# Kernel tuning notes

Hardware: AMD Instinct MI355X
Metric: run time of the kernel (lower is better)

The kernel has to match this reference:

```python
import jax, jax.numpy as jnp
import numpy as np

EMBED_DIM = 1024
NUM_HEADS = 16
HEAD_DIM = EMBED_DIM // NUM_HEADS
B, T = 2, 2048


def setup_inputs() -> dict:
    key = jax.random.key(0)
    ks = jax.random.split(key, 10)
    s_in = 1.0 / np.sqrt(EMBED_DIM)
    s_hd = 1.0 / np.sqrt(HEAD_DIM)
    return {
        "hidden_states": jax.random.normal(ks[0], (B, T, EMBED_DIM), jnp.float32),
        "attn_mask": jnp.zeros((T, T), jnp.float32),
        # per-head parameter stacks (nn.Linear: y = x @ W^T + b); store W pre-transposed
        "W_q": jax.random.uniform(ks[1], (NUM_HEADS, EMBED_DIM, HEAD_DIM), jnp.float32, -s_in, s_in),
        "b_q": jax.random.uniform(ks[2], (NUM_HEADS, HEAD_DIM), jnp.float32, -s_in, s_in),
        "W_k": jax.random.uniform(ks[3], (NUM_HEADS, EMBED_DIM, HEAD_DIM), jnp.float32, -s_in, s_in),
        "b_k": jax.random.uniform(ks[4], (NUM_HEADS, HEAD_DIM), jnp.float32, -s_in, s_in),
        "W_v": jax.random.uniform(ks[5], (NUM_HEADS, EMBED_DIM, HEAD_DIM), jnp.float32, -s_in, s_in),
        "b_v": jax.random.uniform(ks[6], (NUM_HEADS, HEAD_DIM), jnp.float32, -s_in, s_in),
        "W_o": jax.random.uniform(ks[7], (NUM_HEADS, HEAD_DIM, EMBED_DIM), jnp.float32, -s_hd, s_hd),
        "b_o": jax.random.uniform(ks[8], (NUM_HEADS, EMBED_DIM), jnp.float32, -s_hd, s_hd),
        "gate": jnp.ones((NUM_HEADS,), jnp.float32),
    }


def reference(hidden_states, attn_mask, W_q, b_q, W_k, b_k, W_v, b_v, W_o, b_o, gate):
    # All heads: state='active', consent=True (defaults); dropout in eval mode.
    scale = 1.0 / np.sqrt(HEAD_DIM)
    # Q,K,V: [B,H,T,hd]
    Q = jnp.einsum("btd,hde->bhte", hidden_states, W_q) + b_q[None, :, None, :]
    K = jnp.einsum("btd,hde->bhte", hidden_states, W_k) + b_k[None, :, None, :]
    V = jnp.einsum("btd,hde->bhte", hidden_states, W_v) + b_v[None, :, None, :]
    scores = jnp.einsum("bhte,bhse->bhts", Q, K) * scale + attn_mask[None, None, :, :]
    weights = jax.nn.softmax(scores, axis=-1)
    out = jnp.einsum("bhts,bhse->bhte", weights, V)  # [B,H,T,hd]
    # per-head scalar norm: mean over (B,T) of L2 norm along head_dim, floored at 1e-5
    denom = jnp.maximum(
        jnp.sqrt(jnp.sum(out * out, axis=-1)).mean(axis=(0, 2)), 1e-5
    )  # [H]
    out_n = out / denom[None, :, None, None]
    g = jnp.clip(gate, 0.0, 1.0)  # gate_factor = 1.0 for 'active' heads
    # projected per head: (out_n @ W_o + b_o) * g; then sum over heads / H
    proj = (jnp.einsum("bhte,hed->bhtd", out_n, W_o) + b_o[None, :, None, :]) * g[None, :, None, None]
    return proj.sum(axis=1) / NUM_HEADS
```

## Files before the change

kernel.cpp:

```cpp
#include <hip/hip_runtime.h>
#include <hip/hip_bf16.h>
#include <math.h>

#define EMBED_DIM 1024
#define NUM_HEADS 16
#define HEAD_DIM  64
#define B_SZ      2
#define T_SZ      2048
#define BT        (B_SZ * T_SZ)
#define LOG2E     1.44269504088896340736f
#define QSCALE    (0.125f * LOG2E)
#define SOFT_OFF  8.0f

typedef short bf16x8 __attribute__((ext_vector_type(8)));
typedef float f32x4  __attribute__((ext_vector_type(4)));

#define MFMA16(a, b, c) __builtin_amdgcn_mfma_f32_16x16x32_bf16((a), (b), (c), 0, 0, 0)

__device__ inline short f2bf(float f) {
    unsigned u = __builtin_bit_cast(unsigned, f);
    u = (u + 0x7fffu + ((u >> 16) & 1u)) >> 16;
    return (short)u;
}
__device__ inline float bf2f(short s) {
    unsigned u = ((unsigned)(unsigned short)s) << 16;
    return __builtin_bit_cast(float, u);
}
__device__ inline unsigned pk2(float a, float b) {
#if __has_builtin(__builtin_amdgcn_cvt_pk_bf16_f32)
    typedef __bf16 bf2_t __attribute__((ext_vector_type(2)));
    bf2_t t = __builtin_amdgcn_cvt_pk_bf16_f32(a, b);
    return __builtin_bit_cast(unsigned, t);
#else
    return (unsigned)(unsigned short)f2bf(a) | ((unsigned)(unsigned short)f2bf(b) << 16);
#endif
}

__device__ inline float ex2(float x) {
#if __has_builtin(__builtin_amdgcn_exp2f)
    return __builtin_amdgcn_exp2f(x);
#else
    return exp2f(x);
#endif
}

__device__ inline void gld16(const short* g, short* lds) {
    __builtin_amdgcn_global_load_lds(
        (const __attribute__((address_space(1))) void*)g,
        (__attribute__((address_space(3))) void*)lds, 16, 0, 0);
}

__device__ inline bf16x8 frag_swz(const short* tile, int R, int C) {
    return *(const bf16x8*)(tile + R * 64 + ((C ^ (R & 7)) << 3));
}

__device__ inline float red_add64(float v) {
    v += __shfl_xor(v, 1); v += __shfl_xor(v, 2); v += __shfl_xor(v, 4);
    v += __shfl_xor(v, 8); v += __shfl_xor(v, 16); v += __shfl_xor(v, 32);
    return v;
}

__global__ __launch_bounds__(256) void prep_kernel(
    const float* __restrict__ hs, short* __restrict__ hsb,
    const float* __restrict__ maskf, unsigned* __restrict__ flagsW,
    const float* __restrict__ Wq, const float* __restrict__ Wk,
    const float* __restrict__ Wv, const float* __restrict__ Wo,
    short* __restrict__ Wqt, short* __restrict__ Wkt,
    short* __restrict__ Wvt, short* __restrict__ WoT)
{
    __shared__ float tile[32][33];
    const int bx = blockIdx.x, tid = threadIdx.x;

    if (bx < 4096) {
        const long i = ((long)bx * 256 + tid) * 4;
        const float4 v = *(const float4*)(hs + i);
        ushort4 o; o.x = f2bf(v.x); o.y = f2bf(v.y); o.z = f2bf(v.z); o.w = f2bf(v.w);
        *(ushort4*)(hsb + i) = o;
    } else if (bx < 4608) {
        const int flat = bx - 4096;
        const int qc = flat >> 5, kt = flat & 31;
        const float* base = maskf + (long)qc * 128 * 2048 + kt * 64;
        unsigned u = 0;
        #pragma unroll
        for (int i = 0; i < 8; ++i) {
            const int f2 = i * 256 + tid;
            const int r = f2 >> 4, c4 = f2 & 15;
            const uint4 v = *(const uint4*)(base + (long)r * 2048 + c4 * 4);
            u |= v.x | v.y | v.z | v.w;
        }
        if (__any(u != 0) && (tid & 63) == 0)
            atomicOr(&flagsW[qc], 1u << kt);
    } else {
        const int j = bx - 4608;
        const int x = j & 63, rest = j >> 6;
        const int h = rest & 15, arr = rest >> 4;
        const float* src; short* dst; int R, C;
        if (arr == 0)      { src = Wq; dst = Wqt; R = 1024; C = 64; }
        else if (arr == 1) { src = Wk; dst = Wkt; R = 1024; C = 64; }
        else if (arr == 2) { src = Wv; dst = Wvt; R = 1024; C = 64; }
        else               { src = Wo; dst = WoT; R = 64;   C = 1024; }
        src += (long)h * 65536; dst += (long)h * 65536;

        const int ct = C / 32;
        const int tr = x / ct, tc = x % ct;
        const int tx = tid & 31, ty = tid >> 5;
        #pragma unroll
        for (int i = 0; i < 4; ++i) {
            const int r = ty + 8 * i;
            tile[r][tx] = src[(long)(tr * 32 + r) * C + tc * 32 + tx];
        }
        __syncthreads();
        #pragma unroll
        for (int i = 0; i < 4; ++i) {
            const int r = ty + 8 * i;
            dst[(long)(tc * 32 + r) * R + tr * 32 + tx] = f2bf(tile[tx][r]);
        }
    }
}

__global__ __launch_bounds__(256) void qkv_mfma_kernel(
    const short* __restrict__ hsb,
    const short* __restrict__ Wt,
    const float* __restrict__ bq, const float* __restrict__ bk,
    const float* __restrict__ bv,
    short* __restrict__ Qb, short* __restrict__ Kb, short* __restrict__ Vtb)
{
    const int r_ = blockIdx.x;
    const int c_ = r_ & 7, j_ = r_ >> 3;
    const int xi = j_ & 7, yi = j_ >> 3;
    const int m0 = ((c_ & 3) * 8 + xi) * 128;
    const int n0 = ((c_ >> 2) * 12 + yi) * 128;
    const int type = n0 >> 10;

    __shared__ short As[128 * 64];
    __shared__ short Bs[128 * 64];

    const int tid = threadIdx.x, lane = tid & 63, w = tid >> 6;
    const int wm = w & 1, wn = w >> 1;
    const int quad = lane >> 4, l15 = lane & 15;

    f32x4 acc[4][4] = {};

    if (type < 2) {
        for (int k0 = 0; k0 < 1024; k0 += 64) {
            __syncthreads();
            #pragma unroll
            for (int t = 0; t < 4; ++t) {
                const int r0 = w * 32 + t * 8;
                const int r  = r0 + (lane >> 3);
                const int cg = (lane & 7) ^ (r & 7);
                gld16(hsb + (long)(m0 + r) * 1024 + k0 + cg * 8, &As[r0 * 64]);
                gld16(Wt  + (long)(n0 + r) * 1024 + k0 + cg * 8, &Bs[r0 * 64]);
            }
            __syncthreads();
            #pragma unroll
            for (int ks = 0; ks < 2; ++ks) {
                bf16x8 af[4];
                #pragma unroll
                for (int ms = 0; ms < 4; ++ms)
                    af[ms] = frag_swz(As, wm * 64 + ms * 16 + l15, ks * 4 + quad);
                #pragma unroll
                for (int ns = 0; ns < 4; ++ns) {
                    const bf16x8 bfr = frag_swz(Bs, wn * 64 + ns * 16 + l15, ks * 4 + quad);
                    #pragma unroll
                    for (int ms = 0; ms < 4; ++ms)
                        acc[ms][ns] = MFMA16(bfr, af[ms], acc[ms][ns]);
                }
            }
        }

        const int hh = (((n0 + wn * 64) >> 6) & 15);
        const float* bsrc = (type == 0 ? bq : bk) + hh * 64;
        short* dst = (type == 0 ? Qb : Kb);
        const float sc = (type == 0) ? QSCALE : 1.0f;
        #pragma unroll
        for (int ns = 0; ns < 4; ++ns) {
            const int e0 = ns * 16 + quad * 4;
            const float4 b4 = *(const float4*)(bsrc + e0);
            #pragma unroll
            for (int ms = 0; ms < 4; ++ms) {
                const int t  = m0 + wm * 64 + ms * 16 + l15;
                const int bb = t >> 11, t0 = t & 2047;
                ushort4 pk;
                pk.x = (unsigned short)f2bf((acc[ms][ns][0] + b4.x) * sc);
                pk.y = (unsigned short)f2bf((acc[ms][ns][1] + b4.y) * sc);
                pk.z = (unsigned short)f2bf((acc[ms][ns][2] + b4.z) * sc);
                pk.w = (unsigned short)f2bf((acc[ms][ns][3] + b4.w) * sc);
                *(ushort4*)&dst[((long)(bb * 16 + hh) * 2048 + t0) * 64 + e0] = pk;
            }
        }
    } else {
        for (int k0 = 0; k0 < 1024; k0 += 64) {
            __syncthreads();
            #pragma unroll
            for (int t = 0; t < 4; ++t) {
                const int r0 = w * 32 + t * 8;
                const int r  = r0 + (lane >> 3);
                const int cg = (lane & 7) ^ (r & 7);
                gld16(hsb + (long)(m0 + r) * 1024 + k0 + cg * 8, &As[r0 * 64]);
                gld16(Wt  + (long)(n0 + r) * 1024 + k0 + cg * 8, &Bs[r0 * 64]);
            }
            __syncthreads();
            #pragma unroll
            for (int ks = 0; ks < 2; ++ks) {
                bf16x8 af[4];
                #pragma unroll
                for (int ms = 0; ms < 4; ++ms)
                    af[ms] = frag_swz(As, wm * 64 + ms * 16 + l15, ks * 4 + quad);
                #pragma unroll
                for (int ns = 0; ns < 4; ++ns) {
                    const bf16x8 bfr = frag_swz(Bs, wn * 64 + ns * 16 + l15, ks * 4 + quad);
                    #pragma unroll
                    for (int ms = 0; ms < 4; ++ms)
                        acc[ms][ns] = MFMA16(af[ms], bfr, acc[ms][ns]);
                }
            }
        }

        #pragma unroll
        for (int ns = 0; ns < 4; ++ns) {
            const int n = n0 + wn * 64 + ns * 16 + l15;
            const int h = (n >> 6) & 15;
            const int e = n & 63;
            const float bias = bv[h * 64 + e];
            #pragma unroll
            for (int ms = 0; ms < 4; ++ms) {
                const int mbase = m0 + wm * 64 + ms * 16 + quad * 4;
                const int bb = mbase >> 11, t0 = mbase & 2047;
                const int tp = (t0 & ~63) | (t0 & 35) | ((t0 & 12) << 1) | ((t0 & 16) >> 2);
                ushort4 pk;
                pk.x = (unsigned short)f2bf(acc[ms][ns][0] + bias);
                pk.y = (unsigned short)f2bf(acc[ms][ns][1] + bias);
                pk.z = (unsigned short)f2bf(acc[ms][ns][2] + bias);
                pk.w = (unsigned short)f2bf(acc[ms][ns][3] + bias);
                *(ushort4*)&Vtb[((long)(bb * 16 + h) * 64 + e) * 2048 + tp] = pk;
            }
        }
    }
}

__global__ __launch_bounds__(512) void attn_mfma_kernel(
    const short* __restrict__ Qb, const short* __restrict__ Kb,
    const short* __restrict__ Vtb, const float* __restrict__ maskf,
    const unsigned* __restrict__ flagsW,
    short* __restrict__ Ob, float* __restrict__ denomsum)
{
    const int r_  = blockIdx.x;
    const int c_  = r_ & 7, j_ = r_ >> 3;
    const int g_  = c_ + 8 * (j_ >> 4);
    const int qc  = j_ & 15;
    const int q0  = qc * 128;
    const int h   = g_ & 15, b = g_ >> 4;
    const long bh = ((long)b * 16 + h) * (long)T_SZ * 64;

    __shared__ short Ks[2][128 * 64];
    __shared__ short Vs[2][128 * 64];
    __shared__ float wred[8];

    const int tid = threadIdx.x, lane = tid & 63, w = tid >> 6;
    const int quad = lane >> 4, l15 = lane & 15;
    const int qrow = q0 + w * 16 + l15;

    const unsigned zf = flagsW[qc];

    const short* Kg = Kb + bh;
    const short* Vg = Vtb + bh;

    bf16x8 qf[2];
    #pragma unroll
    for (int ks = 0; ks < 2; ++ks)
        qf[ks] = *(const bf16x8*)(Qb + bh + (long)qrow * 64 + ks * 32 + quad * 8);

    bf16x8 ones;
    #pragma unroll
    for (int i = 0; i < 8; ++i) ones[i] = (short)0x3F80;

    f32x4 o[4] = {};
    f32x4 lacc = {};

    const float* mrow = maskf + (long)qrow * 2048 + quad * 4;

    auto stageKV = [&](int st, int buf) {
        const int kv0 = st * 128;
        #pragma unroll
        for (int t = 0; t < 2; ++t) {
            const int r0 = w * 16 + t * 8;
            const int r  = r0 + (lane >> 3);
            const int cg = (lane & 7) ^ (r & 7);
            gld16(Kg + (long)(kv0 + r) * 64 + cg * 8, &Ks[buf][r0 * 64]);
        }
        #pragma unroll
        for (int t = 0; t < 2; ++t) {
            const int r0 = w * 8;
            const int r  = r0 + (lane >> 3);
            const int cg = (lane & 7) ^ (r & 7);
            gld16(Vg + (long)r * 2048 + kv0 + t * 64 + cg * 8,
                  &Vs[buf][t * 4096 + r0 * 64]);
        }
    };

    stageKV(0, 0);

    for (int st = 0; st < 16; ++st) {
        const int cur = st & 1;

        __builtin_amdgcn_s_barrier();
        asm volatile("" ::: "memory");
        if (st < 15) {
            stageKV(st + 1, cur ^ 1);
            asm volatile("s_waitcnt vmcnt(4)" ::: "memory");
        } else {
            asm volatile("s_waitcnt vmcnt(0)" ::: "memory");
        }
        __builtin_amdgcn_s_barrier();
        asm volatile("" ::: "memory");

        #pragma unroll
        for (int k2 = 0; k2 < 2; ++k2) {
            const int kt = st * 2 + k2;
            const short* Kt = &Ks[cur][k2 * 4096];
            const short* Vt = &Vs[cur][k2 * 4096];

            f32x4 s[4];
            if (zf & (1u << kt)) {
                const int kv0 = kt * 64;
                #pragma unroll
                for (int kb = 0; kb < 4; ++kb) {
                    const float4 m = *(const float4*)(mrow + kv0 + kb * 16);
                    s[kb][0] = fmaf(m.x, LOG2E, -SOFT_OFF);
                    s[kb][1] = fmaf(m.y, LOG2E, -SOFT_OFF);
                    s[kb][2] = fmaf(m.z, LOG2E, -SOFT_OFF);
                    s[kb][3] = fmaf(m.w, LOG2E, -SOFT_OFF);
                }
            } else {
                #pragma unroll
                for (int kb = 0; kb < 4; ++kb) {
                    s[kb][0] = -SOFT_OFF; s[kb][1] = -SOFT_OFF;
                    s[kb][2] = -SOFT_OFF; s[kb][3] = -SOFT_OFF;
                }
            }

            __builtin_amdgcn_s_setprio(1);
            #pragma unroll
            for (int ks = 0; ks < 2; ++ks)
                #pragma unroll
                for (int kb = 0; kb < 4; ++kb) {
                    const bf16x8 kf = frag_swz(Kt, kb * 16 + l15, ks * 4 + quad);
                    s[kb] = MFMA16(kf, qf[ks], s[kb]);
                }
            __builtin_amdgcn_s_setprio(0);

            unsigned w0[4], w1[4];
            #pragma unroll
            for (int kb = 0; kb < 4; ++kb) {
                const float p0 = ex2(s[kb][0]);
                const float p1 = ex2(s[kb][1]);
                const float p2 = ex2(s[kb][2]);
                const float p3 = ex2(s[kb][3]);
                w0[kb] = pk2(p0, p1);
                w1[kb] = pk2(p2, p3);
            }

            __builtin_amdgcn_s_setprio(1);
            #pragma unroll
            for (int kbp = 0; kbp < 2; ++kbp) {
                const uint4 u = {w0[2 * kbp], w1[2 * kbp],
                                 w0[2 * kbp + 1], w1[2 * kbp + 1]};
                const bf16x8 pb = __builtin_bit_cast(bf16x8, u);
                lacc = MFMA16(ones, pb, lacc);
                #pragma unroll
                for (int eb = 0; eb < 4; ++eb) {
                    const bf16x8 va = frag_swz(Vt, eb * 16 + l15, kbp * 4 + quad);
                    o[eb] = MFMA16(va, pb, o[eb]);
                }
            }
            __builtin_amdgcn_s_setprio(0);
        }
    }

    const float inv = 1.f / lacc[0];
    float ss = 0.f;
    #pragma unroll
    for (int eb = 0; eb < 4; ++eb) {
        o[eb] *= inv;
        #pragma unroll
        for (int r = 0; r < 4; ++r) ss += o[eb][r] * o[eb][r];
    }
    ss += __shfl_xor(ss, 16);
    ss += __shfl_xor(ss, 32);
    const float tot = sqrtf(ss);

    #pragma unroll
    for (int eb = 0; eb < 4; ++eb) {
        uint2 pk;
        pk.x = pk2(o[eb][0], o[eb][1]);
        pk.y = pk2(o[eb][2], o[eb][3]);
        *(uint2*)&Ob[((long)(b * 2048 + qrow)) * 1024 + h * 64 + eb * 16 + quad * 4] = pk;
    }

    const float wsum = red_add64(tot) * 0.25f;
    if (lane == 0) wred[w] = wsum;
    __syncthreads();
    if (tid == 0) {
        float acc = 0.f;
        #pragma unroll
        for (int i = 0; i < 8; ++i) acc += wred[i];
        atomicAdd(&denomsum[h], acc);
    }
}

__global__ __launch_bounds__(256) void scale_w_kernel(
    short* __restrict__ WoT, const float* __restrict__ denomsum,
    const float* __restrict__ gate)
{
    __shared__ float sh[16];
    if (threadIdx.x < 16) {
        const float g  = fminf(fmaxf(gate[threadIdx.x], 0.f), 1.f);
        const float dn = fmaxf(denomsum[threadIdx.x] * (1.f / (float)BT), 1e-5f);
        sh[threadIdx.x] = g / (dn * (float)NUM_HEADS);
    }
    __syncthreads();
    const long i = ((long)blockIdx.x * 256 + threadIdx.x) * 4;
    const float sc = sh[(int)(i >> 16)];
    ushort4 v = *(ushort4*)(WoT + i);
    v.x = (unsigned short)f2bf(bf2f((short)v.x) * sc);
    v.y = (unsigned short)f2bf(bf2f((short)v.y) * sc);
    v.z = (unsigned short)f2bf(bf2f((short)v.z) * sc);
    v.w = (unsigned short)f2bf(bf2f((short)v.w) * sc);
    *(ushort4*)(WoT + i) = v;
}

__global__ __launch_bounds__(256) void oproj_mfma_kernel(
    const short* __restrict__ Ob,
    const short* __restrict__ WoT,
    const float* __restrict__ bo,
    const float* __restrict__ gate,
    float* __restrict__ out)
{
    const int m0 = blockIdx.x * 64;
    const int n0 = blockIdx.y * 128;
    __shared__ short As[2][64 * 64];
    __shared__ short Bs[2][128 * 64];

    const int tid = threadIdx.x, lane = tid & 63, w = tid >> 6;
    const int wm = w & 1, wn = w >> 1;
    const int quad = lane >> 4, l15 = lane & 15;

    auto stage = [&](int h, int buf) {
        #pragma unroll
        for (int t = 0; t < 2; ++t) {
            const int r0 = w * 16 + t * 8;
            const int r  = r0 + (lane >> 3);
            const int cg = (lane & 7) ^ (r & 7);
            gld16(Ob + (long)(m0 + r) * 1024 + h * 64 + cg * 8, &As[buf][r0 * 64]);
        }
        #pragma unroll
        for (int t = 0; t < 4; ++t) {
            const int r0 = w * 32 + t * 8;
            const int r  = r0 + (lane >> 3);
            const int cg = (lane & 7) ^ (r & 7);
            gld16(WoT + (long)h * 65536 + (long)(n0 + r) * 64 + cg * 8, &Bs[buf][r0 * 64]);
        }
    };

    f32x4 acc[2][4] = {};
    stage(0, 0);

    for (int h = 0; h < 16; ++h) {
        const int cur = h & 1;
        __syncthreads();
        if (h < 15) stage(h + 1, cur ^ 1);
        #pragma unroll
        for (int ks = 0; ks < 2; ++ks) {
            bf16x8 af[2];
            #pragma unroll
            for (int ms = 0; ms < 2; ++ms)
                af[ms] = frag_swz(&As[cur][0], wm * 32 + ms * 16 + l15, ks * 4 + quad);
            #pragma unroll
            for (int ns = 0; ns < 4; ++ns) {
                const bf16x8 bfr = frag_swz(&Bs[cur][0], wn * 64 + ns * 16 + l15, ks * 4 + quad);
                #pragma unroll
                for (int ms = 0; ms < 2; ++ms)
                    acc[ms][ns] = MFMA16(af[ms], bfr, acc[ms][ns]);
            }
        }
    }

    float gcl[16];
    #pragma unroll
    for (int hh = 0; hh < 16; ++hh)
        gcl[hh] = fminf(fmaxf(gate[hh], 0.f), 1.f) * (1.f / (float)NUM_HEADS);

    #pragma unroll
    for (int ns = 0; ns < 4; ++ns) {
        const int n = n0 + wn * 64 + ns * 16 + l15;
        float be = 0.f;
        #pragma unroll
        for (int hh = 0; hh < 16; ++hh) be += gcl[hh] * bo[hh * 1024 + n];
        #pragma unroll
        for (int ms = 0; ms < 2; ++ms) {
            const int m = m0 + wm * 32 + ms * 16 + quad * 4;
            #pragma unroll
            for (int r = 0; r < 4; ++r)
                out[(long)(m + r) * 1024 + n] = acc[ms][ns][r] + be;
        }
    }
}

extern "C" void kernel_launch(void* const* d_in, const int* in_sizes, int n_in,
                              void* d_out, int out_size, void* d_ws, size_t ws_size,
                              hipStream_t stream)
{
    const float* hs   = (const float*)d_in[0];
    const float* mask = (const float*)d_in[1];
    const float* Wq   = (const float*)d_in[2];
    const float* bq   = (const float*)d_in[3];
    const float* Wk   = (const float*)d_in[4];
    const float* bk   = (const float*)d_in[5];
    const float* Wv   = (const float*)d_in[6];
    const float* bv   = (const float*)d_in[7];
    const float* Wo   = (const float*)d_in[8];
    const float* bo   = (const float*)d_in[9];
    const float* gate = (const float*)d_in[10];
    float* out = (float*)d_out;

    char* ws = (char*)d_ws;
    const size_t MB = 1024 * 1024;
    short* hsb   = (short*)(ws);
    short* Wqt   = (short*)(ws + 8  * MB);
    short* Wkt   = (short*)(ws + 10 * MB);
    short* Wvt   = (short*)(ws + 12 * MB);
    short* WoT   = (short*)(ws + 14 * MB);
    short* Qb    = (short*)(ws + 16 * MB);
    short* Kb    = (short*)(ws + 24 * MB);
    short* Vtb   = (short*)(ws + 32 * MB);
    short* Ob    = (short*)(ws + 40 * MB);
    float* denomsum = (float*)(ws + 48 * MB);
    unsigned* flagsW = (unsigned*)(ws + 48 * MB + 4096);

    (void)hipMemsetAsync(denomsum, 0, NUM_HEADS * sizeof(float), stream);
    (void)hipMemsetAsync(flagsW, 0, 16 * sizeof(unsigned), stream);

    prep_kernel<<<8704, 256, 0, stream>>>(
        hs, hsb, mask, flagsW, Wq, Wk, Wv, Wo, Wqt, Wkt, Wvt, WoT);
    qkv_mfma_kernel<<<768, 256, 0, stream>>>(
        hsb, Wqt, bq, bk, bv, Qb, Kb, Vtb);
    attn_mfma_kernel<<<512, 512, 0, stream>>>(
        Qb, Kb, Vtb, mask, flagsW, Ob, denomsum);
    scale_w_kernel<<<1024, 256, 0, stream>>>(WoT, denomsum, gate);
    oproj_mfma_kernel<<<dim3(64, 8), 256, 0, stream>>>(
        Ob, WoT, bo, gate, out);
}
```

Measured before the change: 221.2 us.

## Split attention KV range in two halves and add combine kernel

The attention kernel now splits each query tile's key/value range into two halves, launching twice as many blocks with smaller LDS tiles. Each half writes unnormalized bf16 partial outputs and row sums, and a new combine kernel merges them, normalizes, writes Ob and accumulates the per-head norm sums. The aim is more parallelism and occupancy on the many-CU GPU. The cost is an extra launch, extra global traffic for the partials, and bf16 rounding of the unnormalized partials. Opart reuses the hsb workspace region, which the qkv kernel no longer needs at that point.

```diff
diff --git a/kernel.cpp b/kernel.cpp
--- a/kernel.cpp
+++ b/kernel.cpp
@@ -52,12 +52,6 @@
 
 __device__ inline bf16x8 frag_swz(const short* tile, int R, int C) {
     return *(const bf16x8*)(tile + R * 64 + ((C ^ (R & 7)) << 3));
-}
-
-__device__ inline float red_add64(float v) {
-    v += __shfl_xor(v, 1); v += __shfl_xor(v, 2); v += __shfl_xor(v, 4);
-    v += __shfl_xor(v, 8); v += __shfl_xor(v, 16); v += __shfl_xor(v, 32);
-    return v;
 }
 
 __global__ __launch_bounds__(256) void prep_kernel(
@@ -243,19 +237,21 @@
     const short* __restrict__ Qb, const short* __restrict__ Kb,
     const short* __restrict__ Vtb, const float* __restrict__ maskf,
     const unsigned* __restrict__ flagsW,
-    short* __restrict__ Ob, float* __restrict__ denomsum)
-{
-    const int r_  = blockIdx.x;
-    const int c_  = r_ & 7, j_ = r_ >> 3;
-    const int g_  = c_ + 8 * (j_ >> 4);
-    const int qc  = j_ & 15;
-    const int q0  = qc * 128;
-    const int h   = g_ & 15, b = g_ >> 4;
-    const long bh = ((long)b * 16 + h) * (long)T_SZ * 64;
-
-    __shared__ short Ks[2][128 * 64];
-    __shared__ short Vs[2][128 * 64];
-    __shared__ float wred[8];
+    short* __restrict__ Opart,
+    float* __restrict__ lpart)
+{
+    const int r_   = blockIdx.x;
+    const int c_   = r_ & 7, j_ = r_ >> 3;
+    const int hb   = c_ + 8 * (j_ >> 5);
+    const int qh   = j_ & 31;
+    const int qc   = qh & 15, half = qh >> 4;
+    const int q0   = qc * 128;
+    const int h    = hb & 15, b = hb >> 4;
+    const long bh  = ((long)b * 16 + h) * (long)T_SZ * 64;
+    const int kvbase = half * 1024;
+
+    __shared__ short Ks[2][64 * 64];
+    __shared__ short Vs[2][64 * 64];
 
     const int tid = threadIdx.x, lane = tid & 63, w = tid >> 6;
     const int quad = lane >> 4, l15 = lane & 15;
@@ -278,135 +274,135 @@
     f32x4 o[4] = {};
     f32x4 lacc = {};
 
-    const float* mrow = maskf + (long)qrow * 2048 + quad * 4;
-
-    auto stageKV = [&](int st, int buf) {
-        const int kv0 = st * 128;
-        #pragma unroll
-        for (int t = 0; t < 2; ++t) {
-            const int r0 = w * 16 + t * 8;
-            const int r  = r0 + (lane >> 3);
-            const int cg = (lane & 7) ^ (r & 7);
-            gld16(Kg + (long)(kv0 + r) * 64 + cg * 8, &Ks[buf][r0 * 64]);
-        }
-        #pragma unroll
-        for (int t = 0; t < 2; ++t) {
-            const int r0 = w * 8;
-            const int r  = r0 + (lane >> 3);
-            const int cg = (lane & 7) ^ (r & 7);
-            gld16(Vg + (long)r * 2048 + kv0 + t * 64 + cg * 8,
-                  &Vs[buf][t * 4096 + r0 * 64]);
-        }
+    const float* mrow = maskf + (long)qrow * 2048 + kvbase + quad * 4;
+
+    auto stageKV = [&](int kt, int buf) {
+        const int kv0 = kvbase + kt * 64;
+        const int r0 = w * 8;
+        const int r  = r0 + (lane >> 3);
+        const int cg = (lane & 7) ^ (r & 7);
+        gld16(Kg + (long)(kv0 + r) * 64 + cg * 8, &Ks[buf][r0 * 64]);
+        gld16(Vg + (long)r * 2048 + kv0 + cg * 8, &Vs[buf][r0 * 64]);
     };
 
     stageKV(0, 0);
 
-    for (int st = 0; st < 16; ++st) {
-        const int cur = st & 1;
+    for (int kt = 0; kt < 16; ++kt) {
+        const int cur = kt & 1;
 
         __builtin_amdgcn_s_barrier();
         asm volatile("" ::: "memory");
-        if (st < 15) {
-            stageKV(st + 1, cur ^ 1);
-            asm volatile("s_waitcnt vmcnt(4)" ::: "memory");
+        if (kt < 15) {
+            stageKV(kt + 1, cur ^ 1);
+            asm volatile("s_waitcnt vmcnt(2)" ::: "memory");
         } else {
             asm volatile("s_waitcnt vmcnt(0)" ::: "memory");
         }
         __builtin_amdgcn_s_barrier();
         asm volatile("" ::: "memory");
 
-        #pragma unroll
-        for (int k2 = 0; k2 < 2; ++k2) {
-            const int kt = st * 2 + k2;
-            const short* Kt = &Ks[cur][k2 * 4096];
-            const short* Vt = &Vs[cur][k2 * 4096];
-
-            f32x4 s[4];
-            if (zf & (1u << kt)) {
-                const int kv0 = kt * 64;
-                #pragma unroll
-                for (int kb = 0; kb < 4; ++kb) {
-                    const float4 m = *(const float4*)(mrow + kv0 + kb * 16);
-                    s[kb][0] = fmaf(m.x, LOG2E, -SOFT_OFF);
-                    s[kb][1] = fmaf(m.y, LOG2E, -SOFT_OFF);
-                    s[kb][2] = fmaf(m.z, LOG2E, -SOFT_OFF);
-                    s[kb][3] = fmaf(m.w, LOG2E, -SOFT_OFF);
-                }
-            } else {
-                #pragma unroll
-                for (int kb = 0; kb < 4; ++kb) {
-                    s[kb][0] = -SOFT_OFF; s[kb][1] = -SOFT_OFF;
-                    s[kb][2] = -SOFT_OFF; s[kb][3] = -SOFT_OFF;
-                }
-            }
-
-            __builtin_amdgcn_s_setprio(1);
-            #pragma unroll
-            for (int ks = 0; ks < 2; ++ks)
-                #pragma unroll
-                for (int kb = 0; kb < 4; ++kb) {
-                    const bf16x8 kf = frag_swz(Kt, kb * 16 + l15, ks * 4 + quad);
-                    s[kb] = MFMA16(kf, qf[ks], s[kb]);
-                }
-            __builtin_amdgcn_s_setprio(0);
-
-            unsigned w0[4], w1[4];
+        f32x4 s[4];
+        if (zf & (1u << (half * 16 + kt))) {
+            const int kv0 = kt * 64;
             #pragma unroll
             for (int kb = 0; kb < 4; ++kb) {
-                const float p0 = ex2(s[kb][0]);
-                const float p1 = ex2(s[kb][1]);
-                const float p2 = ex2(s[kb][2]);
-                const float p3 = ex2(s[kb][3]);
-                w0[kb] = pk2(p0, p1);
-                w1[kb] = pk2(p2, p3);
-            }
-
-            __builtin_amdgcn_s_setprio(1);
-            #pragma unroll
-            for (int kbp = 0; kbp < 2; ++kbp) {
-                const uint4 u = {w0[2 * kbp], w1[2 * kbp],
-                                 w0[2 * kbp + 1], w1[2 * kbp + 1]};
-                const bf16x8 pb = __builtin_bit_cast(bf16x8, u);
-                lacc = MFMA16(ones, pb, lacc);
-                #pragma unroll
-                for (int eb = 0; eb < 4; ++eb) {
-                    const bf16x8 va = frag_swz(Vt, eb * 16 + l15, kbp * 4 + quad);
-                    o[eb] = MFMA16(va, pb, o[eb]);
-                }
-            }
-            __builtin_amdgcn_s_setprio(0);
-        }
-    }
-
-    const float inv = 1.f / lacc[0];
-    float ss = 0.f;
-    #pragma unroll
-    for (int eb = 0; eb < 4; ++eb) {
-        o[eb] *= inv;
-        #pragma unroll
-        for (int r = 0; r < 4; ++r) ss += o[eb][r] * o[eb][r];
-    }
-    ss += __shfl_xor(ss, 16);
-    ss += __shfl_xor(ss, 32);
-    const float tot = sqrtf(ss);
-
+                const float4 m = *(const float4*)(mrow + kv0 + kb * 16);
+                s[kb][0] = fmaf(m.x, LOG2E, -SOFT_OFF);
+                s[kb][1] = fmaf(m.y, LOG2E, -SOFT_OFF);
+                s[kb][2] = fmaf(m.z, LOG2E, -SOFT_OFF);
+                s[kb][3] = fmaf(m.w, LOG2E, -SOFT_OFF);
+            }
+        } else {
+            #pragma unroll
+            for (int kb = 0; kb < 4; ++kb) {
+                s[kb][0] = -SOFT_OFF; s[kb][1] = -SOFT_OFF;
+                s[kb][2] = -SOFT_OFF; s[kb][3] = -SOFT_OFF;
+            }
+        }
+
+        __builtin_amdgcn_s_setprio(1);
+        #pragma unroll
+        for (int ks = 0; ks < 2; ++ks)
+            #pragma unroll
+            for (int kb = 0; kb < 4; ++kb) {
+                const bf16x8 kf = frag_swz(&Ks[cur][0], kb * 16 + l15, ks * 4 + quad);
+                s[kb] = MFMA16(kf, qf[ks], s[kb]);
+            }
+        __builtin_amdgcn_s_setprio(0);
+
+        unsigned w0[4], w1[4];
+        #pragma unroll
+        for (int kb = 0; kb < 4; ++kb) {
+            const float p0 = ex2(s[kb][0]);
+            const float p1 = ex2(s[kb][1]);
+            const float p2 = ex2(s[kb][2]);
+            const float p3 = ex2(s[kb][3]);
+            w0[kb] = pk2(p0, p1);
+            w1[kb] = pk2(p2, p3);
+        }
+
+        __builtin_amdgcn_s_setprio(1);
+        #pragma unroll
+        for (int kbp = 0; kbp < 2; ++kbp) {
+            const uint4 u = {w0[2 * kbp], w1[2 * kbp],
+                             w0[2 * kbp + 1], w1[2 * kbp + 1]};
+            const bf16x8 pb = __builtin_bit_cast(bf16x8, u);
+            lacc = MFMA16(ones, pb, lacc);
+            #pragma unroll
+            for (int eb = 0; eb < 4; ++eb) {
+                const bf16x8 va = frag_swz(&Vs[cur][0], eb * 16 + l15, kbp * 4 + quad);
+                o[eb] = MFMA16(va, pb, o[eb]);
+            }
+        }
+        __builtin_amdgcn_s_setprio(0);
+    }
+
+    const long rbase = (long)b * 2048 + qrow;
     #pragma unroll
     for (int eb = 0; eb < 4; ++eb) {
         uint2 pk;
         pk.x = pk2(o[eb][0], o[eb][1]);
         pk.y = pk2(o[eb][2], o[eb][3]);
-        *(uint2*)&Ob[((long)(b * 2048 + qrow)) * 1024 + h * 64 + eb * 16 + quad * 4] = pk;
-    }
-
-    const float wsum = red_add64(tot) * 0.25f;
-    if (lane == 0) wred[w] = wsum;
+        *(uint2*)&Opart[(long)half * (4096 * 1024) + rbase * 1024 +
+                        h * 64 + eb * 16 + quad * 4] = pk;
+    }
+    if (quad == 0)
+        lpart[(long)half * (4096 * 16) + rbase * 16 + h] = lacc[0];
+}
+
+__global__ __launch_bounds__(256) void combine_kernel(
+    const short* __restrict__ Opart,
+    const float* __restrict__ lpart,
+    short* __restrict__ Ob,
+    float* __restrict__ denomsum)
+{
+    __shared__ float hacc[16];
+    const int tid = threadIdx.x;
+    if (tid < 16) hacc[tid] = 0.f;
     __syncthreads();
-    if (tid == 0) {
-        float acc = 0.f;
-        #pragma unroll
-        for (int i = 0; i < 8; ++i) acc += wred[i];
-        atomicAdd(&denomsum[h], acc);
-    }
+    const int h = tid >> 4;
+    const int row0 = blockIdx.x * 8;
+    for (int rr = 0; rr < 8; ++rr) {
+        const int row = row0 + rr;
+        const long base = (long)row * 1024 + tid * 4;
+        const ushort4 a0 = *(const ushort4*)(Opart + base);
+        const ushort4 a1 = *(const ushort4*)(Opart + (long)4096 * 1024 + base);
+        const float l0 = lpart[row * 16 + h];
+        const float l1 = lpart[4096 * 16 + row * 16 + h];
+        const float inv = 1.f / (l0 + l1);
+        const float o0 = (bf2f((short)a0.x) + bf2f((short)a1.x)) * inv;
+        const float o1 = (bf2f((short)a0.y) + bf2f((short)a1.y)) * inv;
+        const float o2 = (bf2f((short)a0.z) + bf2f((short)a1.z)) * inv;
+        const float o3 = (bf2f((short)a0.w) + bf2f((short)a1.w)) * inv;
+        uint2 pk; pk.x = pk2(o0, o1); pk.y = pk2(o2, o3);
+        *(uint2*)(Ob + base) = pk;
+        float ss = (o0 * o0 + o1 * o1) + (o2 * o2 + o3 * o3);
+        ss += __shfl_xor(ss, 1); ss += __shfl_xor(ss, 2);
+        ss += __shfl_xor(ss, 4); ss += __shfl_xor(ss, 8);
+        if ((tid & 15) == 0) atomicAdd(&hacc[h], sqrtf(ss));
+    }
+    __syncthreads();
+    if (tid < 16) atomicAdd(&denomsum[tid], hacc[tid]);
 }
 
 __global__ __launch_bounds__(256) void scale_w_kernel(
@@ -530,13 +526,15 @@
     short* Wqt   = (short*)(ws + 8  * MB);
     short* Wkt   = (short*)(ws + 10 * MB);
     short* Wvt   = (short*)(ws + 12 * MB);
-    short* WoT   = (short*)(ws + 14 * MB);
+    short* Opart = (short*)(ws);
     short* Qb    = (short*)(ws + 16 * MB);
     short* Kb    = (short*)(ws + 24 * MB);
     short* Vtb   = (short*)(ws + 32 * MB);
     short* Ob    = (short*)(ws + 40 * MB);
-    float* denomsum = (float*)(ws + 48 * MB);
-    unsigned* flagsW = (unsigned*)(ws + 48 * MB + 4096);
+    short* WoT   = (short*)(ws + 48 * MB);
+    float* lpart = (float*)(ws + 50 * MB);
+    float* denomsum = (float*)(ws + 51 * MB);
+    unsigned* flagsW = (unsigned*)(ws + 51 * MB + 4096);
 
     (void)hipMemsetAsync(denomsum, 0, NUM_HEADS * sizeof(float), stream);
     (void)hipMemsetAsync(flagsW, 0, 16 * sizeof(unsigned), stream);
@@ -545,8 +543,9 @@
         hs, hsb, mask, flagsW, Wq, Wk, Wv, Wo, Wqt, Wkt, Wvt, WoT);
     qkv_mfma_kernel<<<768, 256, 0, stream>>>(
         hsb, Wqt, bq, bk, bv, Qb, Kb, Vtb);
-    attn_mfma_kernel<<<512, 512, 0, stream>>>(
-        Qb, Kb, Vtb, mask, flagsW, Ob, denomsum);
+    attn_mfma_kernel<<<1024, 512, 0, stream>>>(
+        Qb, Kb, Vtb, mask, flagsW, Opart, lpart);
+    combine_kernel<<<512, 256, 0, stream>>>(Opart, lpart, Ob, denomsum);
     scale_w_kernel<<<1024, 256, 0, stream>>>(WoT, denomsum, gate);
     oproj_mfma_kernel<<<dim3(64, 8), 256, 0, stream>>>(
         Ob, WoT, bo, gate, out);
```

Result: slower. 238.4 us (+7.8%).

## Fold per-head norm scaling into output projection and drop scale_w kernel

Applied to the files above, without the earlier changes.

Removes the separate scale_w_kernel launch, which rescaled the bf16 Wo weights by gate/denominator. The output projection now applies that per-head scale to a per-head partial accumulator inside the K loop. Wo is re-laid out as a single [1024 x 1024] matrix with heads concatenated along K. Block tiling changes from 64x128 to 128x64, and the double-buffered LDS staging is replaced by a single buffer with two barriers per step. This trades the loss of load/compute overlap and extra FMAs per head for one fewer launch and less weight memory traffic.

```diff
diff --git a/kernel.cpp b/kernel.cpp
--- a/kernel.cpp
+++ b/kernel.cpp
@@ -66,7 +66,7 @@
     const float* __restrict__ Wq, const float* __restrict__ Wk,
     const float* __restrict__ Wv, const float* __restrict__ Wo,
     short* __restrict__ Wqt, short* __restrict__ Wkt,
-    short* __restrict__ Wvt, short* __restrict__ WoT)
+    short* __restrict__ Wvt, short* __restrict__ Wo2)
 {
     __shared__ float tile[32][33];
     const int bx = blockIdx.x, tid = threadIdx.x;
@@ -94,12 +94,13 @@
         const int j = bx - 4608;
         const int x = j & 63, rest = j >> 6;
         const int h = rest & 15, arr = rest >> 4;
-        const float* src; short* dst; int R, C;
-        if (arr == 0)      { src = Wq; dst = Wqt; R = 1024; C = 64; }
-        else if (arr == 1) { src = Wk; dst = Wkt; R = 1024; C = 64; }
-        else if (arr == 2) { src = Wv; dst = Wvt; R = 1024; C = 64; }
-        else               { src = Wo; dst = WoT; R = 64;   C = 1024; }
-        src += (long)h * 65536; dst += (long)h * 65536;
+        const float* src; short* dst; int C;
+        if (arr == 0)      { src = Wq; dst = Wqt; C = 64; }
+        else if (arr == 1) { src = Wk; dst = Wkt; C = 64; }
+        else if (arr == 2) { src = Wv; dst = Wvt; C = 64; }
+        else               { src = Wo; dst = Wo2; C = 1024; }
+        src += (long)h * 65536;
+        if (arr != 3) dst += (long)h * 65536;
 
         const int ct = C / 32;
         const int tr = x / ct, tc = x % ct;
@@ -113,7 +114,10 @@
         #pragma unroll
         for (int i = 0; i < 4; ++i) {
             const int r = ty + 8 * i;
-            dst[(long)(tc * 32 + r) * R + tr * 32 + tx] = f2bf(tile[tx][r]);
+            if (arr == 3)
+                dst[(long)(tc * 32 + r) * 1024 + h * 64 + tr * 32 + tx] = f2bf(tile[tx][r]);
+            else
+                dst[(long)(tc * 32 + r) * 1024 + tr * 32 + tx] = f2bf(tile[tx][r]);
         }
     }
 }
@@ -409,97 +413,84 @@
     }
 }
 
-__global__ __launch_bounds__(256) void scale_w_kernel(
-    short* __restrict__ WoT, const float* __restrict__ denomsum,
-    const float* __restrict__ gate)
-{
-    __shared__ float sh[16];
-    if (threadIdx.x < 16) {
-        const float g  = fminf(fmaxf(gate[threadIdx.x], 0.f), 1.f);
-        const float dn = fmaxf(denomsum[threadIdx.x] * (1.f / (float)BT), 1e-5f);
-        sh[threadIdx.x] = g / (dn * (float)NUM_HEADS);
-    }
-    __syncthreads();
-    const long i = ((long)blockIdx.x * 256 + threadIdx.x) * 4;
-    const float sc = sh[(int)(i >> 16)];
-    ushort4 v = *(ushort4*)(WoT + i);
-    v.x = (unsigned short)f2bf(bf2f((short)v.x) * sc);
-    v.y = (unsigned short)f2bf(bf2f((short)v.y) * sc);
-    v.z = (unsigned short)f2bf(bf2f((short)v.z) * sc);
-    v.w = (unsigned short)f2bf(bf2f((short)v.w) * sc);
-    *(ushort4*)(WoT + i) = v;
-}
-
 __global__ __launch_bounds__(256) void oproj_mfma_kernel(
     const short* __restrict__ Ob,
-    const short* __restrict__ WoT,
+    const short* __restrict__ Wo2,
     const float* __restrict__ bo,
     const float* __restrict__ gate,
+    const float* __restrict__ denomsum,
     float* __restrict__ out)
 {
-    const int m0 = blockIdx.x * 64;
-    const int n0 = blockIdx.y * 128;
-    __shared__ short As[2][64 * 64];
-    __shared__ short Bs[2][128 * 64];
+    const int m0 = blockIdx.x * 128;
+    const int n0 = blockIdx.y * 64;
+    __shared__ short As[128 * 64];
+    __shared__ short Bs[64 * 64];
+    __shared__ float sh_s[16], sh_g[16];
 
     const int tid = threadIdx.x, lane = tid & 63, w = tid >> 6;
     const int wm = w & 1, wn = w >> 1;
     const int quad = lane >> 4, l15 = lane & 15;
 
-    auto stage = [&](int h, int buf) {
+    if (tid < 16) {
+        const float g  = fminf(fmaxf(gate[tid], 0.f), 1.f);
+        const float dn = fmaxf(denomsum[tid] * (1.f / (float)BT), 1e-5f);
+        sh_g[tid] = g * (1.f / (float)NUM_HEADS);
+        sh_s[tid] = g / (dn * (float)NUM_HEADS);
+    }
+
+    f32x4 acc[4][2] = {};
+
+    for (int k0 = 0; k0 < 1024; k0 += 64) {
+        const int hh = k0 >> 6;
+        __syncthreads();
+        #pragma unroll
+        for (int t = 0; t < 4; ++t) {
+            const int r0 = w * 32 + t * 8;
+            const int r  = r0 + (lane >> 3);
+            const int cg = (lane & 7) ^ (r & 7);
+            gld16(Ob + (long)(m0 + r) * 1024 + k0 + cg * 8, &As[r0 * 64]);
+        }
         #pragma unroll
         for (int t = 0; t < 2; ++t) {
             const int r0 = w * 16 + t * 8;
             const int r  = r0 + (lane >> 3);
             const int cg = (lane & 7) ^ (r & 7);
-            gld16(Ob + (long)(m0 + r) * 1024 + h * 64 + cg * 8, &As[buf][r0 * 64]);
-        }
-        #pragma unroll
-        for (int t = 0; t < 4; ++t) {
-            const int r0 = w * 32 + t * 8;
-            const int r  = r0 + (lane >> 3);
-            const int cg = (lane & 7) ^ (r & 7);
-            gld16(WoT + (long)h * 65536 + (long)(n0 + r) * 64 + cg * 8, &Bs[buf][r0 * 64]);
-        }
-    };
-
-    f32x4 acc[2][4] = {};
-    stage(0, 0);
-
-    for (int h = 0; h < 16; ++h) {
-        const int cur = h & 1;
+            gld16(Wo2 + (long)(n0 + r) * 1024 + k0 + cg * 8, &Bs[r0 * 64]);
+        }
         __syncthreads();
-        if (h < 15) stage(h + 1, cur ^ 1);
+
+        f32x4 sacc[4][2] = {};
         #pragma unroll
         for (int ks = 0; ks < 2; ++ks) {
-            bf16x8 af[2];
-            #pragma unroll
-            for (int ms = 0; ms < 2; ++ms)
-                af[ms] = frag_swz(&As[cur][0], wm * 32 + ms * 16 + l15, ks * 4 + quad);
-            #pragma unroll
-            for (int ns = 0; ns < 4; ++ns) {
-                const bf16x8 bfr = frag_swz(&Bs[cur][0], wn * 64 + ns * 16 + l15, ks * 4 + quad);
-                #pragma unroll
-                for (int ms = 0; ms < 2; ++ms)
-                    acc[ms][ns] = MFMA16(af[ms], bfr, acc[ms][ns]);
-            }
-        }
-    }
-
-    float gcl[16];
+            bf16x8 af[4];
+            #pragma unroll
+            for (int ms = 0; ms < 4; ++ms)
+                af[ms] = frag_swz(As, wm * 64 + ms * 16 + l15, ks * 4 + quad);
+            #pragma unroll
+            for (int ns = 0; ns < 2; ++ns) {
+                const bf16x8 bfr = frag_swz(Bs, wn * 32 + ns * 16 + l15, ks * 4 + quad);
+                #pragma unroll
+                for (int ms = 0; ms < 4; ++ms)
+                    sacc[ms][ns] = MFMA16(af[ms], bfr, sacc[ms][ns]);
+            }
+        }
+        const float sc = sh_s[hh];
+        #pragma unroll
+        for (int ms = 0; ms < 4; ++ms)
+            #pragma unroll
+            for (int ns = 0; ns < 2; ++ns)
+                acc[ms][ns] += sacc[ms][ns] * sc;
+    }
+
     #pragma unroll
-    for (int hh = 0; hh < 16; ++hh)
-        gcl[hh] = fminf(fmaxf(gate[hh], 0.f), 1.f) * (1.f / (float)NUM_HEADS);
-
-    #pragma unroll
-    for (int ns = 0; ns < 4; ++ns) {
-        const int n = n0 + wn * 64 + ns * 16 + l15;
+    for (int ns = 0; ns < 2; ++ns) {
+        const int n = n0 + wn * 32 + ns * 16 + l15;
         float be = 0.f;
         #pragma unroll
-        for (int hh = 0; hh < 16; ++hh) be += gcl[hh] * bo[hh * 1024 + n];
-        #pragma unroll
-        for (int ms = 0; ms < 2; ++ms) {
-            const int m = m0 + wm * 32 + ms * 16 + quad * 4;
+        for (int hh = 0; hh < 16; ++hh) be += sh_g[hh] * bo[hh * 1024 + n];
+        #pragma unroll
+        for (int ms = 0; ms < 4; ++ms) {
+            const int m = m0 + wm * 64 + ms * 16 + quad * 4;
             #pragma unroll
             for (int r = 0; r < 4; ++r)
                 out[(long)(m + r) * 1024 + n] = acc[ms][ns][r] + be;
@@ -530,7 +521,7 @@
     short* Wqt   = (short*)(ws + 8  * MB);
     short* Wkt   = (short*)(ws + 10 * MB);
     short* Wvt   = (short*)(ws + 12 * MB);
-    short* WoT   = (short*)(ws + 14 * MB);
+    short* Wo2   = (short*)(ws + 14 * MB);
     short* Qb    = (short*)(ws + 16 * MB);
     short* Kb    = (short*)(ws + 24 * MB);
     short* Vtb   = (short*)(ws + 32 * MB);
@@ -542,12 +533,11 @@
     (void)hipMemsetAsync(flagsW, 0, 16 * sizeof(unsigned), stream);
 
     prep_kernel<<<8704, 256, 0, stream>>>(
-        hs, hsb, mask, flagsW, Wq, Wk, Wv, Wo, Wqt, Wkt, Wvt, WoT);
+        hs, hsb, mask, flagsW, Wq, Wk, Wv, Wo, Wqt, Wkt, Wvt, Wo2);
     qkv_mfma_kernel<<<768, 256, 0, stream>>>(
         hsb, Wqt, bq, bk, bv, Qb, Kb, Vtb);
     attn_mfma_kernel<<<512, 512, 0, stream>>>(
         Qb, Kb, Vtb, mask, flagsW, Ob, denomsum);
-    scale_w_kernel<<<1024, 256, 0, stream>>>(WoT, denomsum, gate);
-    oproj_mfma_kernel<<<dim3(64, 8), 256, 0, stream>>>(
-        Ob, WoT, bo, gate, out);
-}
+    oproj_mfma_kernel<<<dim3(32, 16), 256, 0, stream>>>(
+        Ob, Wo2, bo, gate, denomsum, out);
+}
```

Result: no change. 220.1 us (-0.5%).
